# Kernel optimization log

Hardware: AMD Instinct MI355X
Metric: run time of the kernel (lower is better)

The kernel has to match this reference:

```python
import jax, jax.numpy as jnp
import numpy as np

FOCAL = 1015.0
IMG = 256


def setup_inputs() -> dict:
    key = jax.random.key(0)
    ks = jax.random.split(key, 9)
    B, NV, NF = 128, 35709, 70789
    coeff = jax.random.normal(ks[0], (B, 257), jnp.float32) * 0.1
    meanshape = jax.random.normal(ks[1], (NV * 3,), jnp.float32)
    idBase = jax.random.normal(ks[2], (NV * 3, 80), jnp.float32) * 0.01
    exBase = jax.random.normal(ks[3], (NV * 3, 64), jnp.float32) * 0.01
    meantex = jax.random.uniform(ks[4], (NV * 3,), jnp.float32) * 255.0
    texBase = jax.random.normal(ks[5], (NV * 3, 80), jnp.float32)
    # 1-based indices, matching the facemodel convention (code subtracts 1)
    tri = jax.random.randint(ks[6], (NF, 3), 1, NV + 1, jnp.int32)
    # point_buf may reference the appended zero face (index NF+1, 1-based)
    point_buf = jax.random.randint(ks[7], (NV, 8), 1, NF + 2, jnp.int32)
    kp_inds = jax.random.randint(ks[8], (68,), 0, NV, jnp.int32)
    return dict(coeff=coeff, meanshape=meanshape, idBase=idBase, exBase=exBase,
                meantex=meantex, texBase=texBase, tri=tri, point_buf=point_buf,
                kp_inds=kp_inds)


def _rotation(angles):
    # rotation = (Rz @ Ry @ Rx)^T, per Compute_rotation_matrix
    sx, sy, sz = jnp.sin(angles[:, 0]), jnp.sin(angles[:, 1]), jnp.sin(angles[:, 2])
    cx, cy, cz = jnp.cos(angles[:, 0]), jnp.cos(angles[:, 1]), jnp.cos(angles[:, 2])
    o, l = jnp.zeros_like(sx), jnp.ones_like(sx)
    Rx = jnp.stack([l, o, o, o, cx, -sx, o, sx, cx], -1).reshape(-1, 3, 3)
    Ry = jnp.stack([cy, o, sy, o, l, o, -sy, o, cy], -1).reshape(-1, 3, 3)
    Rz = jnp.stack([cz, -sz, o, sz, cz, o, o, o, l], -1).reshape(-1, 3, 3)
    return jnp.einsum('bij,bjk,bkl->bli', Rz, Ry, Rx)


def _compute_norm(shape, tri, point_buf):
    fid = tri - 1  # [F,3] 0-based vertex ids
    v1 = shape[:, fid[:, 0]]  # [B,F,3]
    v2 = shape[:, fid[:, 1]]
    v3 = shape[:, fid[:, 2]]
    fn = jnp.cross(v1 - v2, v2 - v3)  # per-face normals [B,F,3]
    fn = jnp.concatenate([fn, jnp.zeros_like(fn[:, :1])], axis=1)  # pad zero face
    vn = fn[:, point_buf - 1].sum(axis=2)  # [B,NV,8,3] -> [B,NV,3]
    return vn / jnp.linalg.norm(vn, axis=2, keepdims=True)


def _illumination(tex, norm, gamma):
    B, N, _ = tex.shape
    gamma = gamma.reshape(B, 3, 9).at[:, :, 0].add(0.8).transpose(0, 2, 1)  # [B,9,3]
    a0 = np.pi
    a1 = 2.0 * np.pi / np.sqrt(3.0)
    a2 = 2.0 * np.pi / np.sqrt(8.0)
    c0 = 1.0 / np.sqrt(4.0 * np.pi)
    c1 = np.sqrt(3.0) / np.sqrt(4.0 * np.pi)
    c2 = 3.0 * np.sqrt(5.0) / np.sqrt(12.0 * np.pi)
    d0 = 0.5 / np.sqrt(3.0)
    nx, ny, nz = norm[..., 0], norm[..., 1], norm[..., 2]
    Y = jnp.stack([
        jnp.full_like(nx, np.float32(a0 * c0)),
        -a1 * c1 * ny,
        a1 * c1 * nz,
        -a1 * c1 * nx,
        a2 * c2 * nx * ny,
        -a2 * c2 * ny * nz,
        a2 * c2 * d0 * (3.0 * nz ** 2 - 1.0),
        -a2 * c2 * nx * nz,
        a2 * c2 * 0.5 * (nx ** 2 - ny ** 2),
    ], axis=-1)  # [B,N,9]
    lighting = jnp.einsum('bnc,bcd->bnd', Y, gamma)  # [B,N,3]
    return tex * lighting


def _project(pts):
    half = IMG // 2
    pts = pts * jnp.array([1.0, 1.0, -1.0], jnp.float32) + jnp.array([0.0, 0.0, 10.0], jnp.float32)
    P = jnp.array([[FOCAL, 0.0, half], [0.0, FOCAL, half], [0.0, 0.0, 1.0]], jnp.float32)
    aug = pts @ P.T
    return aug[..., :2] / aug[..., 2:3]


def reference(coeff, meanshape, idBase, exBase, meantex, texBase, tri, point_buf, kp_inds):
    B = coeff.shape[0]
    idc, exc, texc = coeff[:, :80], coeff[:, 80:144], coeff[:, 144:224]
    angles, gamma, trans = coeff[:, 224:227], coeff[:, 227:254], coeff[:, 254:257]
    # Shape_formation
    shape = (idc @ idBase.T + exc @ exBase.T + meanshape).reshape(B, -1, 3)
    shape = shape - meanshape.reshape(1, -1, 3).mean(axis=1, keepdims=True)
    # Texture_formation
    tex = (texc @ texBase.T + meantex).reshape(B, -1, 3)
    # Normals, rotation, rigid transform
    vnorm = _compute_norm(shape, tri, point_buf)
    rot = _rotation(angles)  # [B,3,3]
    vnorm_r = jnp.einsum('bnc,bcd->bnd', vnorm, rot)
    shape_t = jnp.einsum('bnc,bcd->bnd', shape, rot) + trans[:, None, :]
    # Illumination (vertex colors) and landmark projection
    face_color = _illumination(tex, vnorm_r, gamma)
    lms = _project(shape_t[:, kp_inds])
    lms = jnp.stack([lms[..., 0], IMG - lms[..., 1]], axis=-1)
    return face_color, lms, shape_t
```

## Files before the change

### kernel.cpp

```cpp
#include <hip/hip_runtime.h>

typedef unsigned short u16;
typedef unsigned int u32;
typedef __attribute__((ext_vector_type(8))) short bfrag;
typedef __attribute__((ext_vector_type(4))) float ffrag;
typedef __attribute__((ext_vector_type(4))) float f4;
typedef __attribute__((ext_vector_type(2))) float f2;
typedef __attribute__((ext_vector_type(4))) int i4;
typedef __attribute__((ext_vector_type(4))) _Float16 h4;

#define NVERT 35709
#define NFACE 70789
#define NV3   107127
#define NB    128

#define SHAPE_OFF 0ull
#define TEX_OFF   54849024ull
#define FQ_OFF    82273536ull
#define CPACK_OFF 154761472ull
#define ROT_OFF   154827008ull
#define G_OFF     154831616ull
#define TRANS_OFF 154845440ull
#define MEAN_OFF  154846976ull
#define PART_OFF  154847040ull

#define LMS_BASE  13712256ull
#define ST_BASE   13729664ull

__device__ __forceinline__ float b2f(u16 s) {
  union { unsigned u; float f; } v; v.u = ((unsigned)s) << 16; return v.f;
}
__device__ __forceinline__ u16 f2b(float x) {
  union { float f; unsigned u; } v; v.f = x;
  unsigned r = v.u + 0x7FFFu + ((v.u >> 16) & 1u);
  return (u16)(r >> 16);
}
__device__ __forceinline__ bfrag cvt8nt(const float* p) {
  f4 a = __builtin_nontemporal_load((const f4*)p);
  f4 b = __builtin_nontemporal_load((const f4*)(p + 4));
  bfrag r;
  r[0] = (short)f2b(a.x); r[1] = (short)f2b(a.y); r[2] = (short)f2b(a.z); r[3] = (short)f2b(a.w);
  r[4] = (short)f2b(b.x); r[5] = (short)f2b(b.y); r[6] = (short)f2b(b.z); r[7] = (short)f2b(b.w);
  return r;
}

__global__ __launch_bounds__(256) void k_mean(const float* __restrict__ ms, float* __restrict__ part) {
  __shared__ float s[3];
  if (threadIdx.x < 3) s[threadIdx.x] = 0.f;
  __syncthreads();
  float a0 = 0.f, a1 = 0.f, a2 = 0.f;
  for (int v = blockIdx.x * 256 + threadIdx.x; v < NVERT; v += 64 * 256) {
    a0 += ms[v * 3 + 0];
    a1 += ms[v * 3 + 1];
    a2 += ms[v * 3 + 2];
  }
  atomicAdd(&s[0], a0); atomicAdd(&s[1], a1); atomicAdd(&s[2], a2);
  __syncthreads();
  if (threadIdx.x < 3) part[blockIdx.x * 3 + threadIdx.x] = s[threadIdx.x];
}

__global__ __launch_bounds__(128) void k_params(const float* __restrict__ coeff, u16* __restrict__ cpack,
                                                float* __restrict__ rot, float* __restrict__ G,
                                                float* __restrict__ tr, const float* __restrict__ part,
                                                float* __restrict__ mean) {
  int b = threadIdx.x;
  if (b < 3) {
    float s = 0.f;
    for (int i = 0; i < 64; i++) s += part[i * 3 + b];
    mean[b] = s * (1.0f / (float)NVERT);
  }
  const float* c = coeff + b * 257;
  u16* cp = cpack + b * 256;
  for (int k = 0; k < 80; k++) cp[k] = f2b(c[k]);
  for (int k = 80; k < 96; k++) cp[k] = 0;
  for (int k = 0; k < 64; k++) cp[96 + k] = f2b(c[80 + k]);
  for (int k = 0; k < 80; k++) cp[160 + k] = f2b(c[144 + k]);
  for (int k = 240; k < 256; k++) cp[k] = 0;
  float ax = c[224], ay = c[225], az = c[226];
  float sx = sinf(ax), cx = cosf(ax);
  float sy = sinf(ay), cy = cosf(ay);
  float sz = sinf(az), cz = cosf(az);
  float* M = rot + b * 9;
  M[0] = cz * cy;  M[1] = cz * sy * sx - sz * cx;  M[2] = sz * sx + cz * sy * cx;
  M[3] = sz * cy;  M[4] = cz * cx + sz * sy * sx;  M[5] = sz * sy * cx - cz * sx;
  M[6] = -sy;      M[7] = cy * sx;                 M[8] = cy * cx;
  float* g = G + b * 27;
  for (int cc = 0; cc < 9; cc++)
    for (int d = 0; d < 3; d++)
      g[cc * 3 + d] = c[227 + d * 9 + cc] + (cc == 0 ? 0.8f : 0.0f);
  float* t = tr + b * 3;
  t[0] = c[254]; t[1] = c[255]; t[2] = c[256];
}

__global__ __launch_bounds__(256) void k_gemm(const float* __restrict__ idB, const float* __restrict__ exB,
                                              const float* __restrict__ txB, const float* __restrict__ ms,
                                              const float* __restrict__ mt, const u16* __restrict__ cpack,
                                              const float* __restrict__ meanc,
                                              float* __restrict__ shp, u16* __restrict__ texo) {
  __shared__ f2  sT[4][128];
  __shared__ u32 tT[4][128];
  int wave = threadIdx.x >> 6, lane = threadIdx.x & 63;
  int jt = blockIdx.x * 4 + wave;
  int col = lane & 15, quad = lane >> 4;
  int j = jt * 16 + col;
  bool jv = (j < NV3);
  int jc = jv ? j : (NV3 - 1);
  bfrag z8 = {0, 0, 0, 0, 0, 0, 0, 0};
  bfrag bid[3], bex[2], btx[3];
  const float* rowI = idB + (size_t)jc * 80;
  const float* rowT = txB + (size_t)jc * 80;
  const float* rowE = exB + (size_t)jc * 64;
#pragma unroll
  for (int f = 0; f < 3; f++) {
    int k = f * 32 + quad * 8;
    bool ok = (k < 80);
    int ks = ok ? k : 0;
    bfrag vi = cvt8nt(rowI + ks);
    bfrag vt = cvt8nt(rowT + ks);
    bid[f] = ok ? vi : z8;
    btx[f] = ok ? vt : z8;
  }
#pragma unroll
  for (int f = 0; f < 2; f++) {
    int k = f * 32 + quad * 8;
    bex[f] = cvt8nt(rowE + k);
  }
  float msj = ms[jc];
  float mtj = mt[jc];
  float mc = meanc[jc % 3];

  float* sw = (float*)&sT[wave][0];
  u32* tw = &tT[wave][0];
  int s0 = quad >> 1;
  int rbase = (quad & 1) << 2;
  int sbase = s0 * 128 + col * 8 + rbase;

  for (int bt = 0; bt < 8; bt++) {
    const u16* cp = cpack + (size_t)(bt * 16 + col) * 256;
    ffrag accS = {0.f, 0.f, 0.f, 0.f};
    ffrag accT = {0.f, 0.f, 0.f, 0.f};
#pragma unroll
    for (int f = 0; f < 3; f++) {
      bfrag a = *(const bfrag*)(cp + f * 32 + quad * 8);
      accS = __builtin_amdgcn_mfma_f32_16x16x32_bf16(a, bid[f], accS, 0, 0, 0);
    }
#pragma unroll
    for (int f = 0; f < 2; f++) {
      bfrag a = *(const bfrag*)(cp + 96 + f * 32 + quad * 8);
      accS = __builtin_amdgcn_mfma_f32_16x16x32_bf16(a, bex[f], accS, 0, 0, 0);
    }
#pragma unroll
    for (int f = 0; f < 3; f++) {
      bfrag a = *(const bfrag*)(cp + 160 + f * 32 + quad * 8);
      accT = __builtin_amdgcn_mfma_f32_16x16x32_bf16(a, btx[f], accT, 0, 0, 0);
    }
#pragma unroll
    for (int rr = 0; rr < 2; rr++) {
      f2 v2;
      v2.x = accS[2 * rr] + msj - mc;
      v2.y = accS[2 * rr + 1] + msj - mc;
      *(f2*)&sw[sbase + 2 * rr] = v2;
      tw[(sbase >> 1) + rr] = (u32)f2b(accT[2 * rr] + mtj) |
                              ((u32)f2b(accT[2 * rr + 1] + mtj) << 16);
    }
#pragma unroll
    for (int s2 = 0; s2 < 2; s2++) {
      int o = lane << 1;
      int j2 = jt * 16 + (o >> 3);
      if (j2 < NV3) {
        size_t sb = (size_t)(bt * 2 + s2) * (size_t)(NV3 * 8);
        f2 vv = sT[wave][s2 * 64 + lane];
        __builtin_nontemporal_store(vv, (f2*)(shp + sb + (size_t)(jt * 128 + o)));
        u32 tv = tT[wave][s2 * 64 + lane];
        __builtin_nontemporal_store(tv, (u32*)(texo + sb + (size_t)(jt * 128 + o)));
      }
    }
  }
}

#define FN_CH2 2213
__global__ __launch_bounds__(256) void k_fn(const float* __restrict__ shpT, const int* __restrict__ tri,
                                            h4* __restrict__ fq) {
  int g = blockIdx.x;
  int xcd = g & 7, sgi = g >> 3;
  int btg = sgi / FN_CH2, chunk = sgi - btg * FN_CH2;
  int bt8 = btg * 8 + xcd;
  int t = threadIdx.x;
  int bi = t & 7, foff = t >> 3;
  int f = chunk * 32 + foff;
  if (f >= NFACE) return;
  int i0 = __builtin_nontemporal_load(tri + f * 3 + 0) - 1;
  int i1 = __builtin_nontemporal_load(tri + f * 3 + 1) - 1;
  int i2 = __builtin_nontemporal_load(tri + f * 3 + 2) - 1;
  const float* sl = shpT + (size_t)bt8 * (size_t)(NV3 * 8);
  int a0 = i0 * 24 + bi, a1 = i1 * 24 + bi, a2 = i2 * 24 + bi;
  float x1 = sl[a0], y1 = sl[a0 + 8], z1 = sl[a0 + 16];
  float x2 = sl[a1], y2 = sl[a1 + 8], z2 = sl[a1 + 16];
  float x3 = sl[a2], y3 = sl[a2 + 8], z3 = sl[a2 + 16];
  float e1x = x1 - x2, e1y = y1 - y2, e1z = z1 - z2;
  float e2x = x2 - x3, e2y = y2 - y3, e2z = z2 - z3;
  h4 st;
  st.x = (_Float16)(e1y * e2z - e1z * e2y);
  st.y = (_Float16)(e1z * e2x - e1x * e2z);
  st.z = (_Float16)(e1x * e2y - e1y * e2x);
  st.w = (_Float16)0.f;
  __builtin_nontemporal_store(st, fq + (size_t)bt8 * (size_t)(NFACE * 8) + (size_t)f * 8 + bi);
}

#define FI_CH2 1116
__global__ __launch_bounds__(256) void k_final(const float* __restrict__ shpT, const u16* __restrict__ texT,
                                               const h4* __restrict__ fq, const int* __restrict__ pbuf,
                                               const float* __restrict__ rot, const float* __restrict__ G,
                                               const float* __restrict__ tr, float* __restrict__ out) {
  __shared__ float scol[8][100];
  __shared__ float sst[8][100];
  int g = blockIdx.x;
  int xcd = g & 7, sgi = g >> 3;
  int btg = sgi / FI_CH2, chunk = sgi - btg * FI_CH2;
  int bt8 = btg * 8 + xcd;
  int t = threadIdx.x;
  int bi = t & 7, voff = t >> 3;
  int v0 = chunk * 32;
  int v = v0 + voff;
  int vc = v < NVERT ? v : NVERT - 1;
  bool valid = v < NVERT;
  int b = bt8 * 8 + bi;
  i4 p0 = *(const i4*)(pbuf + (size_t)vc * 8);
  i4 p1 = *(const i4*)(pbuf + (size_t)vc * 8 + 4);
  int idx[8] = {p0.x, p0.y, p0.z, p0.w, p1.x, p1.y, p1.z, p1.w};
  const h4* fb = fq + (size_t)bt8 * (size_t)(NFACE * 8);
  float vx = 0.f, vy = 0.f, vz = 0.f;
#pragma unroll
  for (int i = 0; i < 8; i++) {
    int id = idx[i] - 1;
    if (id < NFACE) {
      h4 q = fb[(size_t)id * 8 + bi];
      vx += (float)q.x; vy += (float)q.y; vz += (float)q.z;
    }
  }
  float n2 = vx * vx + vy * vy + vz * vz;
  float inv = rsqrtf(fmaxf(n2, 1e-30f));
  vx *= inv; vy *= inv; vz *= inv;
  const float* M = rot + b * 9;
  float nx = vx * M[0] + vy * M[1] + vz * M[2];
  float ny = vx * M[3] + vy * M[4] + vz * M[5];
  float nz = vx * M[6] + vy * M[7] + vz * M[8];
  const float* sl = shpT + (size_t)bt8 * (size_t)(NV3 * 8) + (size_t)vc * 24 + bi;
  float sx = __builtin_nontemporal_load(sl);
  float sy = __builtin_nontemporal_load(sl + 8);
  float sz = __builtin_nontemporal_load(sl + 16);
  const float* T = tr + b * 3;
  float ox = sx * M[0] + sy * M[1] + sz * M[2] + T[0];
  float oy = sx * M[3] + sy * M[4] + sz * M[5] + T[1];
  float oz = sx * M[6] + sy * M[7] + sz * M[8] + T[2];
  const float kc1 = 1.7724539f;
  const float kc2 = 2.4270324f;
  const float kd0 = 0.28867513f;
  float Y[9];
  Y[0] = 0.8862269f;
  Y[1] = -kc1 * ny;
  Y[2] = kc1 * nz;
  Y[3] = -kc1 * nx;
  Y[4] = kc2 * nx * ny;
  Y[5] = -kc2 * ny * nz;
  Y[6] = kc2 * kd0 * (3.f * nz * nz - 1.f);
  Y[7] = -kc2 * nx * nz;
  Y[8] = kc2 * 0.5f * (nx * nx - ny * ny);
  const float* gg = G + b * 27;
  const u16* tp = texT + (size_t)bt8 * (size_t)(NV3 * 8) + (size_t)vc * 24 + bi;
  if (valid) {
#pragma unroll
    for (int d = 0; d < 3; d++) {
      float L = 0.f;
#pragma unroll
      for (int cc = 0; cc < 9; cc++) L += Y[cc] * gg[cc * 3 + d];
      float tx = b2f(__builtin_nontemporal_load(tp + d * 8));
      scol[bi][voff * 3 + d] = tx * L;
    }
    sst[bi][voff * 3 + 0] = ox;
    sst[bi][voff * 3 + 1] = oy;
    sst[bi][voff * 3 + 2] = oz;
  }
  __syncthreads();
  int nvv = NVERT - v0;
  int lim = (nvv < 32 ? nvv : 32) * 3;
  size_t base = (size_t)(bt8 * 8) * NV3 + (size_t)v0 * 3;
#pragma unroll
  for (int it = 0; it < 3; it++) {
    int l = it * 256 + t;
    int b2 = l / 96, e = l - b2 * 96;
    if (e < lim) {
      size_t o = base + (size_t)b2 * NV3 + e;
      __builtin_nontemporal_store(scol[b2][e], out + o);
      __builtin_nontemporal_store(sst[b2][e], out + ST_BASE + o);
    }
  }
}

__global__ __launch_bounds__(128) void k_lms(const float* __restrict__ shpT, const int* __restrict__ kp,
                                             const float* __restrict__ rot, const float* __restrict__ tr,
                                             float* __restrict__ out) {
  int t = threadIdx.x;
  int b = blockIdx.x;
  if (t >= 68) return;
  int v = kp[t];
  const float* sl = shpT + (size_t)(b >> 3) * (size_t)(NV3 * 8) + (size_t)v * 24 + (b & 7);
  float sx = sl[0], sy = sl[8], sz = sl[16];
  const float* M = rot + b * 9;
  const float* T = tr + b * 3;
  float ox = sx * M[0] + sy * M[1] + sz * M[2] + T[0];
  float oy = sx * M[3] + sy * M[4] + sz * M[5] + T[1];
  float oz = sx * M[6] + sy * M[7] + sz * M[8] + T[2];
  float w = 10.f - oz;
  float invw = 1.0f / w;
  float lx = 1015.f * ox * invw + 128.f;
  float ly = 1015.f * oy * invw + 128.f;
  size_t o = LMS_BASE + ((size_t)b * 68 + t) * 2;
  out[o + 0] = lx;
  out[o + 1] = 256.f - ly;
}

extern "C" void kernel_launch(void* const* d_in, const int* in_sizes, int n_in,
                              void* d_out, int out_size, void* d_ws, size_t ws_size,
                              hipStream_t stream) {
  const float* coeff     = (const float*)d_in[0];
  const float* meanshape = (const float*)d_in[1];
  const float* idB       = (const float*)d_in[2];
  const float* exB       = (const float*)d_in[3];
  const float* meantex   = (const float*)d_in[4];
  const float* txB       = (const float*)d_in[5];
  const int* tri         = (const int*)d_in[6];
  const int* pbuf        = (const int*)d_in[7];
  const int* kp          = (const int*)d_in[8];
  float* out = (float*)d_out;
  char* ws = (char*)d_ws;
  float* shpT = (float*)(ws + SHAPE_OFF);
  u16* texT   = (u16*)(ws + TEX_OFF);
  h4* fq      = (h4*)(ws + FQ_OFF);
  u16* cpack  = (u16*)(ws + CPACK_OFF);
  float* rot  = (float*)(ws + ROT_OFF);
  float* G    = (float*)(ws + G_OFF);
  float* tr   = (float*)(ws + TRANS_OFF);
  float* mean = (float*)(ws + MEAN_OFF);
  float* part = (float*)(ws + PART_OFF);

  k_mean<<<64, 256, 0, stream>>>(meanshape, part);
  k_params<<<1, 128, 0, stream>>>(coeff, cpack, rot, G, tr, part, mean);
  k_gemm<<<1674, 256, 0, stream>>>(idB, exB, txB, meanshape, meantex, cpack, mean, shpT, texT);
  k_fn<<<8 * 2 * FN_CH2, 256, 0, stream>>>(shpT, tri, fq);
  k_final<<<8 * 2 * FI_CH2, 256, 0, stream>>>(shpT, texT, fq, pbuf, rot, G, tr, out);
  k_lms<<<128, 128, 0, stream>>>(shpT, kp, rot, tr, out);
}
```

Before: 441.6 us.

## Split shape and texture GEMMs and fuse rigid transform into shape GEMM

New measurement: 420.1 us. 4.9% less time.

```diff
diff --git a/kernel.cpp b/kernel.cpp
--- a/kernel.cpp
+++ b/kernel.cpp
@@ -18,11 +18,10 @@
 #define TEX_OFF   54849024ull
 #define FQ_OFF    82273536ull
 #define CPACK_OFF 154761472ull
-#define ROT_OFF   154827008ull
-#define G_OFF     154831616ull
-#define TRANS_OFF 154845440ull
+#define MPAD_OFF  154827008ull
+#define GG_OFF    154833152ull
 #define MEAN_OFF  154846976ull
-#define PART_OFF  154847040ull
+#define PART_OFF  154846992ull
 
 #define LMS_BASE  13712256ull
 #define ST_BASE   13729664ull
@@ -34,6 +33,9 @@
   union { float f; unsigned u; } v; v.f = x;
   unsigned r = v.u + 0x7FFFu + ((v.u >> 16) & 1u);
   return (u16)(r >> 16);
+}
+__device__ __forceinline__ f4 ld4u(const float* p) {
+  f4 r; __builtin_memcpy(&r, p, 16); return r;
 }
 __device__ __forceinline__ bfrag cvt8nt(const float* p) {
   f4 a = __builtin_nontemporal_load((const f4*)p);
@@ -60,9 +62,8 @@
 }
 
 __global__ __launch_bounds__(128) void k_params(const float* __restrict__ coeff, u16* __restrict__ cpack,
-                                                float* __restrict__ rot, float* __restrict__ G,
-                                                float* __restrict__ tr, const float* __restrict__ part,
-                                                float* __restrict__ mean) {
+                                                float* __restrict__ mpad, float* __restrict__ G,
+                                                const float* __restrict__ part, float* __restrict__ mean) {
   int b = threadIdx.x;
   if (b < 3) {
     float s = 0.f;
@@ -80,97 +81,158 @@
   float sx = sinf(ax), cx = cosf(ax);
   float sy = sinf(ay), cy = cosf(ay);
   float sz = sinf(az), cz = cosf(az);
-  float* M = rot + b * 9;
-  M[0] = cz * cy;  M[1] = cz * sy * sx - sz * cx;  M[2] = sz * sx + cz * sy * cx;
-  M[3] = sz * cy;  M[4] = cz * cx + sz * sy * sx;  M[5] = sz * sy * cx - cz * sx;
-  M[6] = -sy;      M[7] = cy * sx;                 M[8] = cy * cx;
+  float* mp = mpad + b * 12;
+  mp[0] = cz * cy;  mp[1] = cz * sy * sx - sz * cx;  mp[2] = sz * sx + cz * sy * cx;
+  mp[3] = sz * cy;  mp[4] = cz * cx + sz * sy * sx;  mp[5] = sz * sy * cx - cz * sx;
+  mp[6] = -sy;      mp[7] = cy * sx;                 mp[8] = cy * cx;
+  mp[9] = c[254]; mp[10] = c[255]; mp[11] = c[256];
   float* g = G + b * 27;
   for (int cc = 0; cc < 9; cc++)
     for (int d = 0; d < 3; d++)
       g[cc * 3 + d] = c[227 + d * 9 + cc] + (cc == 0 ? 0.8f : 0.0f);
-  float* t = tr + b * 3;
-  t[0] = c[254]; t[1] = c[255]; t[2] = c[256];
-}
-
-__global__ __launch_bounds__(256) void k_gemm(const float* __restrict__ idB, const float* __restrict__ exB,
-                                              const float* __restrict__ txB, const float* __restrict__ ms,
-                                              const float* __restrict__ mt, const u16* __restrict__ cpack,
-                                              const float* __restrict__ meanc,
-                                              float* __restrict__ shp, u16* __restrict__ texo) {
-  __shared__ f2  sT[4][128];
+}
+
+#define SBLK 558
+__global__ __launch_bounds__(256) void k_gemmS(const float* __restrict__ idB, const float* __restrict__ exB,
+                                               const float* __restrict__ ms, const u16* __restrict__ cpack,
+                                               const float* __restrict__ meanc, const float* __restrict__ mpad,
+                                               float* __restrict__ shp, float* __restrict__ out) {
+  __shared__ float SW[4][2][384];
+  int wave = threadIdx.x >> 6, lane = threadIdx.x & 63;
+  int col = lane & 15, quad = lane >> 4;
+  int jb = (blockIdx.x * 4 + wave) * 48;
+  bfrag z8 = {0, 0, 0, 0, 0, 0, 0, 0};
+  bfrag bid[3][3], bex[3][2];
+  float msj[3], mcv[3];
+#pragma unroll
+  for (int T = 0; T < 3; T++) {
+    int j = jb + T * 16 + col;
+    int jc = j < NV3 ? j : NV3 - 1;
+    const float* rowI = idB + (size_t)jc * 80;
+    const float* rowE = exB + (size_t)jc * 64;
+#pragma unroll
+    for (int f = 0; f < 3; f++) {
+      int k = f * 32 + quad * 8;
+      bool ok = (k < 80);
+      int ks = ok ? k : 0;
+      bfrag vi = cvt8nt(rowI + ks);
+      bid[T][f] = ok ? vi : z8;
+    }
+#pragma unroll
+    for (int f = 0; f < 2; f++) bex[T][f] = cvt8nt(rowE + f * 32 + quad * 8);
+    msj[T] = ms[jc];
+    mcv[T] = meanc[jc % 3];
+  }
+  float (*SWl)[384] = SW[wave];
+  int s0 = quad >> 1;
+  int rb = (quad & 1) << 2;
+  int vb = jb / 3;
+  int ilim = NV3 - jb; ilim = (ilim > 48 ? 48 : ilim) * 8;
+  int vlim = NVERT - vb; vlim = vlim > 16 ? 16 : vlim;
+
+  for (int bt = 0; bt < 8; bt++) {
+    const u16* cp = cpack + (size_t)(bt * 16 + col) * 256;
+#pragma unroll
+    for (int T = 0; T < 3; T++) {
+      ffrag acc = {0.f, 0.f, 0.f, 0.f};
+#pragma unroll
+      for (int f = 0; f < 3; f++) {
+        bfrag a = *(const bfrag*)(cp + f * 32 + quad * 8);
+        acc = __builtin_amdgcn_mfma_f32_16x16x32_bf16(a, bid[T][f], acc, 0, 0, 0);
+      }
+#pragma unroll
+      for (int f = 0; f < 2; f++) {
+        bfrag a = *(const bfrag*)(cp + 96 + f * 32 + quad * 8);
+        acc = __builtin_amdgcn_mfma_f32_16x16x32_bf16(a, bex[T][f], acc, 0, 0, 0);
+      }
+#pragma unroll
+      for (int rr = 0; rr < 2; rr++) {
+        f2 v2;
+        v2.x = acc[2 * rr] + msj[T] - mcv[T];
+        v2.y = acc[2 * rr + 1] + msj[T] - mcv[T];
+        *(f2*)&SWl[s0][(T * 16 + col) * 8 + rb + 2 * rr] = v2;
+      }
+    }
+#pragma unroll
+    for (int s = 0; s < 2; s++) {
+      size_t sb = (size_t)(bt * 2 + s) * (size_t)(NV3 * 8) + (size_t)jb * 8;
+#pragma unroll
+      for (int it = 0; it < 3; it++) {
+        int i = it * 128 + lane * 2;
+        if (i < ilim) {
+          f2 vv = *(f2*)&SWl[s][i];
+          __builtin_nontemporal_store(vv, (f2*)(shp + sb + i));
+        }
+      }
+    }
+#pragma unroll
+    for (int s = 0; s < 2; s++) {
+#pragma unroll
+      for (int kk = 0; kk < 2; kk++) {
+        int bi = (lane >> 4) + (kk << 2);
+        int vloc = lane & 15;
+        int b = bt * 16 + s * 8 + bi;
+        float x = SWl[s][vloc * 24 + bi];
+        float y = SWl[s][vloc * 24 + 8 + bi];
+        float z = SWl[s][vloc * 24 + 16 + bi];
+        const float* mp = mpad + b * 12;
+        f4 m0 = *(const f4*)mp;
+        f4 m1 = *(const f4*)(mp + 4);
+        f4 m2 = *(const f4*)(mp + 8);
+        if (vloc < vlim) {
+          float ox = x * m0.x + y * m0.y + z * m0.z + m2.y;
+          float oy = x * m0.w + y * m1.x + z * m1.y + m2.z;
+          float oz = x * m1.z + y * m1.w + z * m2.x + m2.w;
+          size_t o = ST_BASE + (size_t)b * NV3 + (size_t)(vb + vloc) * 3;
+          __builtin_nontemporal_store(ox, out + o);
+          __builtin_nontemporal_store(oy, out + o + 1);
+          __builtin_nontemporal_store(oz, out + o + 2);
+        }
+      }
+    }
+  }
+}
+
+__global__ __launch_bounds__(256) void k_gemmT(const float* __restrict__ txB, const float* __restrict__ mt,
+                                               const u16* __restrict__ cpack, u16* __restrict__ texo) {
   __shared__ u32 tT[4][128];
   int wave = threadIdx.x >> 6, lane = threadIdx.x & 63;
   int jt = blockIdx.x * 4 + wave;
   int col = lane & 15, quad = lane >> 4;
   int j = jt * 16 + col;
-  bool jv = (j < NV3);
-  int jc = jv ? j : (NV3 - 1);
+  int jc = j < NV3 ? j : NV3 - 1;
   bfrag z8 = {0, 0, 0, 0, 0, 0, 0, 0};
-  bfrag bid[3], bex[2], btx[3];
-  const float* rowI = idB + (size_t)jc * 80;
+  bfrag btx[3];
   const float* rowT = txB + (size_t)jc * 80;
-  const float* rowE = exB + (size_t)jc * 64;
 #pragma unroll
   for (int f = 0; f < 3; f++) {
     int k = f * 32 + quad * 8;
     bool ok = (k < 80);
     int ks = ok ? k : 0;
-    bfrag vi = cvt8nt(rowI + ks);
     bfrag vt = cvt8nt(rowT + ks);
-    bid[f] = ok ? vi : z8;
     btx[f] = ok ? vt : z8;
   }
-#pragma unroll
-  for (int f = 0; f < 2; f++) {
-    int k = f * 32 + quad * 8;
-    bex[f] = cvt8nt(rowE + k);
-  }
-  float msj = ms[jc];
   float mtj = mt[jc];
-  float mc = meanc[jc % 3];
-
-  float* sw = (float*)&sT[wave][0];
   u32* tw = &tT[wave][0];
-  int s0 = quad >> 1;
-  int rbase = (quad & 1) << 2;
-  int sbase = s0 * 128 + col * 8 + rbase;
+  int slot = (quad >> 1) * 64 + col * 4 + (quad & 1) * 2;
 
   for (int bt = 0; bt < 8; bt++) {
     const u16* cp = cpack + (size_t)(bt * 16 + col) * 256;
-    ffrag accS = {0.f, 0.f, 0.f, 0.f};
     ffrag accT = {0.f, 0.f, 0.f, 0.f};
-#pragma unroll
-    for (int f = 0; f < 3; f++) {
-      bfrag a = *(const bfrag*)(cp + f * 32 + quad * 8);
-      accS = __builtin_amdgcn_mfma_f32_16x16x32_bf16(a, bid[f], accS, 0, 0, 0);
-    }
-#pragma unroll
-    for (int f = 0; f < 2; f++) {
-      bfrag a = *(const bfrag*)(cp + 96 + f * 32 + quad * 8);
-      accS = __builtin_amdgcn_mfma_f32_16x16x32_bf16(a, bex[f], accS, 0, 0, 0);
-    }
 #pragma unroll
     for (int f = 0; f < 3; f++) {
       bfrag a = *(const bfrag*)(cp + 160 + f * 32 + quad * 8);
       accT = __builtin_amdgcn_mfma_f32_16x16x32_bf16(a, btx[f], accT, 0, 0, 0);
     }
 #pragma unroll
-    for (int rr = 0; rr < 2; rr++) {
-      f2 v2;
-      v2.x = accS[2 * rr] + msj - mc;
-      v2.y = accS[2 * rr + 1] + msj - mc;
-      *(f2*)&sw[sbase + 2 * rr] = v2;
-      tw[(sbase >> 1) + rr] = (u32)f2b(accT[2 * rr] + mtj) |
-                              ((u32)f2b(accT[2 * rr + 1] + mtj) << 16);
-    }
+    for (int rr = 0; rr < 2; rr++)
+      tw[slot + rr] = (u32)f2b(accT[2 * rr] + mtj) | ((u32)f2b(accT[2 * rr + 1] + mtj) << 16);
 #pragma unroll
     for (int s2 = 0; s2 < 2; s2++) {
       int o = lane << 1;
       int j2 = jt * 16 + (o >> 3);
       if (j2 < NV3) {
         size_t sb = (size_t)(bt * 2 + s2) * (size_t)(NV3 * 8);
-        f2 vv = sT[wave][s2 * 64 + lane];
-        __builtin_nontemporal_store(vv, (f2*)(shp + sb + (size_t)(jt * 128 + o)));
         u32 tv = tT[wave][s2 * 64 + lane];
         __builtin_nontemporal_store(tv, (u32*)(texo + sb + (size_t)(jt * 128 + o)));
       }
@@ -189,9 +251,9 @@
   int bi = t & 7, foff = t >> 3;
   int f = chunk * 32 + foff;
   if (f >= NFACE) return;
-  int i0 = __builtin_nontemporal_load(tri + f * 3 + 0) - 1;
-  int i1 = __builtin_nontemporal_load(tri + f * 3 + 1) - 1;
-  int i2 = __builtin_nontemporal_load(tri + f * 3 + 2) - 1;
+  int i0 = tri[f * 3 + 0] - 1;
+  int i1 = tri[f * 3 + 1] - 1;
+  int i2 = tri[f * 3 + 2] - 1;
   const float* sl = shpT + (size_t)bt8 * (size_t)(NV3 * 8);
   int a0 = i0 * 24 + bi, a1 = i1 * 24 + bi, a2 = i2 * 24 + bi;
   float x1 = sl[a0], y1 = sl[a0 + 8], z1 = sl[a0 + 16];
@@ -204,16 +266,14 @@
   st.y = (_Float16)(e1z * e2x - e1x * e2z);
   st.z = (_Float16)(e1x * e2y - e1y * e2x);
   st.w = (_Float16)0.f;
-  __builtin_nontemporal_store(st, fq + (size_t)bt8 * (size_t)(NFACE * 8) + (size_t)f * 8 + bi);
+  fq[(size_t)bt8 * (size_t)(NFACE * 8) + (size_t)f * 8 + bi] = st;
 }
 
 #define FI_CH2 1116
-__global__ __launch_bounds__(256) void k_final(const float* __restrict__ shpT, const u16* __restrict__ texT,
-                                               const h4* __restrict__ fq, const int* __restrict__ pbuf,
-                                               const float* __restrict__ rot, const float* __restrict__ G,
-                                               const float* __restrict__ tr, float* __restrict__ out) {
+__global__ __launch_bounds__(256) void k_final(const u16* __restrict__ texT, const h4* __restrict__ fq,
+                                               const int* __restrict__ pbuf, const float* __restrict__ mpad,
+                                               const float* __restrict__ G, float* __restrict__ out) {
   __shared__ float scol[8][100];
-  __shared__ float sst[8][100];
   int g = blockIdx.x;
   int xcd = g & 7, sgi = g >> 3;
   int btg = sgi / FI_CH2, chunk = sgi - btg * FI_CH2;
@@ -241,18 +301,13 @@
   float n2 = vx * vx + vy * vy + vz * vz;
   float inv = rsqrtf(fmaxf(n2, 1e-30f));
   vx *= inv; vy *= inv; vz *= inv;
-  const float* M = rot + b * 9;
-  float nx = vx * M[0] + vy * M[1] + vz * M[2];
-  float ny = vx * M[3] + vy * M[4] + vz * M[5];
-  float nz = vx * M[6] + vy * M[7] + vz * M[8];
-  const float* sl = shpT + (size_t)bt8 * (size_t)(NV3 * 8) + (size_t)vc * 24 + bi;
-  float sx = __builtin_nontemporal_load(sl);
-  float sy = __builtin_nontemporal_load(sl + 8);
-  float sz = __builtin_nontemporal_load(sl + 16);
-  const float* T = tr + b * 3;
-  float ox = sx * M[0] + sy * M[1] + sz * M[2] + T[0];
-  float oy = sx * M[3] + sy * M[4] + sz * M[5] + T[1];
-  float oz = sx * M[6] + sy * M[7] + sz * M[8] + T[2];
+  const float* mp = mpad + b * 12;
+  f4 m0 = *(const f4*)mp;
+  f4 m1 = *(const f4*)(mp + 4);
+  float m8 = mp[8];
+  float nx = vx * m0.x + vy * m0.y + vz * m0.z;
+  float ny = vx * m0.w + vy * m1.x + vz * m1.y;
+  float nz = vx * m1.z + vy * m1.w + vz * m8;
   const float kc1 = 1.7724539f;
   const float kc2 = 2.4270324f;
   const float kd0 = 0.28867513f;
@@ -267,19 +322,22 @@
   Y[7] = -kc2 * nx * nz;
   Y[8] = kc2 * 0.5f * (nx * nx - ny * ny);
   const float* gg = G + b * 27;
+  float gv[28];
+#pragma unroll
+  for (int q = 0; q < 7; q++) {
+    f4 g4 = ld4u(gg + q * 4);
+    gv[q * 4] = g4.x; gv[q * 4 + 1] = g4.y; gv[q * 4 + 2] = g4.z; gv[q * 4 + 3] = g4.w;
+  }
   const u16* tp = texT + (size_t)bt8 * (size_t)(NV3 * 8) + (size_t)vc * 24 + bi;
   if (valid) {
 #pragma unroll
     for (int d = 0; d < 3; d++) {
       float L = 0.f;
 #pragma unroll
-      for (int cc = 0; cc < 9; cc++) L += Y[cc] * gg[cc * 3 + d];
+      for (int cc = 0; cc < 9; cc++) L += Y[cc] * gv[cc * 3 + d];
       float tx = b2f(__builtin_nontemporal_load(tp + d * 8));
       scol[bi][voff * 3 + d] = tx * L;
     }
-    sst[bi][voff * 3 + 0] = ox;
-    sst[bi][voff * 3 + 1] = oy;
-    sst[bi][voff * 3 + 2] = oz;
   }
   __syncthreads();
   int nvv = NVERT - v0;
@@ -292,25 +350,25 @@
     if (e < lim) {
       size_t o = base + (size_t)b2 * NV3 + e;
       __builtin_nontemporal_store(scol[b2][e], out + o);
-      __builtin_nontemporal_store(sst[b2][e], out + ST_BASE + o);
     }
   }
 }
 
 __global__ __launch_bounds__(128) void k_lms(const float* __restrict__ shpT, const int* __restrict__ kp,
-                                             const float* __restrict__ rot, const float* __restrict__ tr,
-                                             float* __restrict__ out) {
+                                             const float* __restrict__ mpad, float* __restrict__ out) {
   int t = threadIdx.x;
   int b = blockIdx.x;
   if (t >= 68) return;
   int v = kp[t];
   const float* sl = shpT + (size_t)(b >> 3) * (size_t)(NV3 * 8) + (size_t)v * 24 + (b & 7);
   float sx = sl[0], sy = sl[8], sz = sl[16];
-  const float* M = rot + b * 9;
-  const float* T = tr + b * 3;
-  float ox = sx * M[0] + sy * M[1] + sz * M[2] + T[0];
-  float oy = sx * M[3] + sy * M[4] + sz * M[5] + T[1];
-  float oz = sx * M[6] + sy * M[7] + sz * M[8] + T[2];
+  const float* mp = mpad + b * 12;
+  f4 m0 = *(const f4*)mp;
+  f4 m1 = *(const f4*)(mp + 4);
+  f4 m2 = *(const f4*)(mp + 8);
+  float ox = sx * m0.x + sy * m0.y + sz * m0.z + m2.y;
+  float oy = sx * m0.w + sy * m1.x + sz * m1.y + m2.z;
+  float oz = sx * m1.z + sy * m1.w + sz * m2.x + m2.w;
   float w = 10.f - oz;
   float invw = 1.0f / w;
   float lx = 1015.f * ox * invw + 128.f;
@@ -338,16 +396,16 @@
   u16* texT   = (u16*)(ws + TEX_OFF);
   h4* fq      = (h4*)(ws + FQ_OFF);
   u16* cpack  = (u16*)(ws + CPACK_OFF);
-  float* rot  = (float*)(ws + ROT_OFF);
-  float* G    = (float*)(ws + G_OFF);
-  float* tr   = (float*)(ws + TRANS_OFF);
+  float* mpad = (float*)(ws + MPAD_OFF);
+  float* G    = (float*)(ws + GG_OFF);
   float* mean = (float*)(ws + MEAN_OFF);
   float* part = (float*)(ws + PART_OFF);
 
   k_mean<<<64, 256, 0, stream>>>(meanshape, part);
-  k_params<<<1, 128, 0, stream>>>(coeff, cpack, rot, G, tr, part, mean);
-  k_gemm<<<1674, 256, 0, stream>>>(idB, exB, txB, meanshape, meantex, cpack, mean, shpT, texT);
+  k_params<<<1, 128, 0, stream>>>(coeff, cpack, mpad, G, part, mean);
+  k_gemmS<<<SBLK, 256, 0, stream>>>(idB, exB, meanshape, cpack, mean, mpad, shpT, out);
+  k_gemmT<<<1674, 256, 0, stream>>>(txB, meantex, cpack, texT);
   k_fn<<<8 * 2 * FN_CH2, 256, 0, stream>>>(shpT, tri, fq);
-  k_final<<<8 * 2 * FI_CH2, 256, 0, stream>>>(shpT, texT, fq, pbuf, rot, G, tr, out);
-  k_lms<<<128, 128, 0, stream>>>(shpT, kp, rot, tr, out);
-}
+  k_final<<<8 * 2 * FI_CH2, 256, 0, stream>>>(texT, fq, pbuf, mpad, G, out);
+  k_lms<<<128, 128, 0, stream>>>(shpT, kp, mpad, out);
+}
```
